# Optimization experiments

Hardware: AMD Instinct MI355X
Metric: run time of the kernel (lower is better)

The kernel has to match this reference:

```python
import jax, jax.numpy as jnp
import numpy as np

N = 100000   # nodes
E = 1600000  # edges
IN = 3       # in_channels
H = 32       # hidden_channels
C = 10       # num_classes_dynamic (== num output classes here)
G = 64       # number of graphs in the batch


def setup_inputs() -> dict:
    key = jax.random.key(0)
    ks = jax.random.split(key, 12)
    def w(k, shape, fan_in):
        return jax.random.normal(k, shape, jnp.float32) / np.sqrt(fan_in).astype(np.float32)
    inp = {}
    inp["x"] = jax.random.normal(ks[0], (N, IN), jnp.float32)
    inp["edge_index"] = jax.random.randint(ks[1], (2, E), 0, N, jnp.int32)
    inp["batch"] = jnp.sort(jax.random.randint(ks[2], (N,), 0, G, jnp.int32))
    # per-class linear filters (DynamicEdgeConv.filters)
    inp["filt_W"] = w(ks[3], (C, IN, H), IN)
    inp["filt_b"] = jnp.zeros((C, H), jnp.float32)
    # shared edge MLP: Linear(2H,H) -> ReLU -> Linear(H,H)
    inp["mlp_W1"] = w(ks[4], (2 * H, H), 2 * H)
    inp["mlp_b1"] = jnp.zeros((H,), jnp.float32)
    inp["mlp_W2"] = w(ks[5], (H, H), H)
    inp["mlp_b2"] = jnp.zeros((H,), jnp.float32)
    # GCN layers (gcn1 input dim hardcoded 323 = IN + C*H)
    inp["gcn1_W"] = w(ks[6], (IN + C * H, H), IN + C * H)
    inp["gcn1_b"] = jnp.zeros((H,), jnp.float32)
    inp["gcn2_W"] = w(ks[7], (H, H), H)
    inp["gcn2_b"] = jnp.zeros((H,), jnp.float32)
    # classifier
    inp["cls_W"] = w(ks[8], (H, C), H)
    inp["cls_b"] = jnp.zeros((C,), jnp.float32)
    return inp


def _gcn_conv(x, W, b, row, col, dinv):
    # PyG GCNConv: add self-loops, sym-normalize, aggregate src->dst
    xw = x @ W                                   # [N, H]
    norm = dinv[row] * dinv[col]                 # [E]
    out = jax.ops.segment_sum(xw[row] * norm[:, None], col, num_segments=x.shape[0])
    out = out + xw * (dinv * dinv)[:, None]      # self-loop term, norm = 1/deg_i
    return out + b


def _forward(x, edge_index, batch, filt_W, filt_b, mlp_W1, mlp_b1, mlp_W2, mlp_b2,
             gcn1_W, gcn1_b, gcn2_W, gcn2_b, cls_W, cls_b):
    row, col = edge_index[0], edge_index[1]
    n = x.shape[0]

    # DynamicEdgeConv: per-class filter -> gather(row,col) -> edge MLP -> scatter_add into col
    def per_class(_, wb):
        Wc, bc = wb
        xc = x @ Wc + bc                                      # [N, H]
        ef = jnp.concatenate([xc[row], xc[col]], axis=1)      # [E, 2H]
        h = jax.nn.relu(ef @ mlp_W1 + mlp_b1) @ mlp_W2 + mlp_b2
        return None, jax.ops.segment_sum(h, col, num_segments=n)
    _, aggs = jax.lax.scan(per_class, None, (filt_W, filt_b))  # [C, N, H]

    feat = jnp.concatenate([x, aggs.transpose(1, 0, 2).reshape(n, -1)], axis=1)  # [N, IN + C*H]

    deg = jax.ops.segment_sum(jnp.ones(row.shape[0], x.dtype), col, num_segments=n) + 1.0
    dinv = deg ** -0.5
    h1 = jax.nn.relu(_gcn_conv(feat, gcn1_W, gcn1_b, row, col, dinv))
    h2 = jax.nn.relu(_gcn_conv(h1, gcn2_W, gcn2_b, row, col, dinv))

    counts = jax.ops.segment_sum(jnp.ones(n, x.dtype), batch, num_segments=G)
    pooled = jax.ops.segment_sum(h2, batch, num_segments=G) / jnp.maximum(counts, 1.0)[:, None]
    return pooled @ cls_W + cls_b                             # [G, C]


def reference(x, edge_index, batch, filt_W, filt_b, mlp_W1, mlp_b1, mlp_W2, mlp_b2,
              gcn1_W, gcn1_b, gcn2_W, gcn2_b, cls_W, cls_b):
    return _forward(x, edge_index, batch, filt_W, filt_b, mlp_W1, mlp_b1, mlp_W2, mlp_b2,
                    gcn1_W, gcn1_b, gcn2_W, gcn2_b, cls_W, cls_b)
```

## Files before the change

kernel.cpp:

```cpp
#include <hip/hip_runtime.h>

#define NN 100000
#define NE 1600000
#define HH 32
#define CC 10
#define GG 64
#define NB 391
#define PBLK 100
#define ECH 16000
#define MTOT (NB * PBLK)
#define MSB ((MTOT + 255) / 256)

typedef _Float16 half8 __attribute__((ext_vector_type(8)));
typedef _Float16 half2v __attribute__((ext_vector_type(2)));
typedef float f32x4 __attribute__((ext_vector_type(4)));

__global__ void zero_f(float* p, int n) {
    int i = blockIdx.x * 256 + threadIdx.x;
    if (i < n) p[i] = 0.0f;
}

__global__ void precompute_small(const float* __restrict__ fW, const float* __restrict__ fb,
                                 const float* __restrict__ W1, const float* __restrict__ b1,
                                 const float* __restrict__ W2, const float* __restrict__ b2,
                                 const float* __restrict__ g1W, float* __restrict__ tab) {
    int c = blockIdx.x;
    int k = threadIdx.x >> 5;
    int j = threadIdx.x & 31;
    float m = 0.f;
    for (int mm = 0; mm < 32; ++mm)
        m += W2[k * 32 + mm] * g1W[(3 + 32 * c + mm) * 32 + j];
    tab[2240 + c * 1024 + k * 32 + j] = m;

    if (k < 3) {
        float a = 0.f, b = 0.f;
        for (int i = 0; i < 32; ++i) {
            float w = fW[c * 96 + k * 32 + i];
            a += w * W1[i * 32 + j];
            b += w * W1[(32 + i) * 32 + j];
        }
        tab[c * 96 + k * 32 + j] = a;
        tab[960 + c * 96 + k * 32 + j] = b;
    } else if (k == 3) {
        float h = b1[j];
        for (int i = 0; i < 32; ++i)
            h += fb[c * 32 + i] * (W1[i * 32 + j] + W1[(32 + i) * 32 + j]);
        tab[1920 + c * 32 + j] = h;
    } else if (k == 4 && c == 0) {
        float t = 0.f;
        for (int cc2 = 0; cc2 < CC; ++cc2)
            for (int mm = 0; mm < 32; ++mm)
                t += b2[mm] * g1W[(3 + 32 * cc2 + mm) * 32 + j];
        tab[12480 + j] = t;
    }
}

__global__ void mfrag_kernel(const float* __restrict__ tab, _Float16* __restrict__ Mfrag) {
    int gid = blockIdx.x * 256 + threadIdx.x;
    if (gid >= 1280) return;
    int set = gid >> 6, l = gid & 63;
    int kc = set >> 1, jt = set & 1;
    int j = jt * 16 + (l & 15);
    int kbase = kc * 32 + (l >> 4) * 8;
#pragma unroll
    for (int i = 0; i < 8; ++i)
        Mfrag[gid * 8 + i] = (_Float16)tab[2240 + (kbase + i) * 32 + j];
}

__global__ void bucket_hist(const int* __restrict__ ei, int* __restrict__ mat) {
    __shared__ int h[NB];
    int blk = blockIdx.x, tid = threadIdx.x;
    for (int i = tid; i < NB; i += 256) h[i] = 0;
    __syncthreads();
    int base = blk * ECH;
    for (int k = tid; k < ECH; k += 256)
        atomicAdd(&h[ei[NE + base + k] >> 8], 1);
    __syncthreads();
    for (int i = tid; i < NB; i += 256) mat[i * PBLK + blk] = h[i];
}

__global__ void scan_m1(const int* __restrict__ mat, int* __restrict__ msum) {
    __shared__ int sh[256];
    int b = blockIdx.x, t = threadIdx.x;
    int i = b * 256 + t;
    sh[t] = (i < MTOT) ? mat[i] : 0;
    __syncthreads();
    for (int off = 128; off > 0; off >>= 1) {
        if (t < off) sh[t] += sh[t + off];
        __syncthreads();
    }
    if (t == 0) msum[b] = sh[0];
}

__global__ void scan_m2(int* __restrict__ msum) {
    __shared__ int sh[256];
    int t = threadIdx.x;
    int v = (t < MSB) ? msum[t] : 0;
    sh[t] = v;
    __syncthreads();
    for (int off = 1; off < 256; off <<= 1) {
        int add = (t >= off) ? sh[t - off] : 0;
        __syncthreads();
        sh[t] += add;
        __syncthreads();
    }
    if (t < MSB) msum[t] = sh[t] - v;
}

__global__ void scan_m3(int* __restrict__ mat, const int* __restrict__ msum) {
    __shared__ int sh[256];
    int b = blockIdx.x, t = threadIdx.x;
    int i = b * 256 + t;
    int v = (i < MTOT) ? mat[i] : 0;
    sh[t] = v;
    __syncthreads();
    for (int off = 1; off < 256; off <<= 1) {
        int add = (t >= off) ? sh[t - off] : 0;
        __syncthreads();
        sh[t] += add;
        __syncthreads();
    }
    if (i < MTOT) mat[i] = sh[t] - v + msum[b];
}

__global__ void bucket_scatter(const int* __restrict__ ei, const int* __restrict__ mat,
                               unsigned int* __restrict__ part) {
    __shared__ int bas[NB];
    __shared__ int cur[NB];
    int blk = blockIdx.x, tid = threadIdx.x;
    for (int i = tid; i < NB; i += 256) { bas[i] = mat[i * PBLK + blk]; cur[i] = 0; }
    __syncthreads();
    int base = blk * ECH;
    for (int k = tid; k < ECH; k += 256) {
        int e = base + k;
        int r = ei[e];
        int c = ei[NE + e];
        int b = c >> 8;
        int local = atomicAdd(&cur[b], 1);
        part[bas[b] + local] = (unsigned)r | ((unsigned)(c & 255) << 24);
    }
}

__global__ void bucket_build(const unsigned int* __restrict__ part, const int* __restrict__ mat,
                             const float* __restrict__ x, int* __restrict__ csr_row,
                             int* __restrict__ ideg, int* __restrict__ offs,
                             float* __restrict__ dinv, float4* __restrict__ xpad) {
    __shared__ int lh[256];
    __shared__ int lex[256];
    __shared__ int cur[256];
    int b = blockIdx.x, tid = threadIdx.x;
    int ebase = mat[b * PBLK];
    int eend = (b == NB - 1) ? NE : mat[(b + 1) * PBLK];
    int m = eend - ebase;
    lh[tid] = 0;
    __syncthreads();
    for (int k = tid; k < m; k += 256) {
        unsigned v = part[ebase + k];
        atomicAdd(&lh[v >> 24], 1);
    }
    __syncthreads();
    int cnt = lh[tid];
    lex[tid] = cnt;
    __syncthreads();
    for (int off = 1; off < 256; off <<= 1) {
        int v = (tid >= off) ? lex[tid - off] : 0;
        __syncthreads();
        lex[tid] += v;
        __syncthreads();
    }
    int excl = lex[tid] - cnt;
    lex[tid] = excl;
    cur[tid] = 0;
    int n = b * 256 + tid;
    if (n < NN) {
        ideg[n] = cnt;
        offs[n] = ebase + excl;
        float di = rsqrtf((float)cnt + 1.0f);
        dinv[n] = di;
        xpad[n] = make_float4(x[n * 3], x[n * 3 + 1], x[n * 3 + 2], di);
    }
    if (b == 0 && tid == 0) offs[NN] = NE;
    __syncthreads();
    for (int k = tid; k < m; k += 256) {
        unsigned v = part[ebase + k];
        int cl = (int)(v >> 24);
        int r = (int)(v & 0x00FFFFFFu);
        int local = atomicAdd(&cur[cl], 1);
        csr_row[ebase + lex[cl] + local] = r;
    }
}

__device__ __forceinline__ float bcast_lane(float v, int t) {
    return __uint_as_float(__builtin_amdgcn_readlane(__float_as_uint(v), (unsigned)t));
}

__global__ __launch_bounds__(256, 8) void edgeconv_fused(
    const float4* __restrict__ xpad, const int* __restrict__ offs,
    const int* __restrict__ csr_row, const float* __restrict__ tab,
    _Float16* __restrict__ aggh) {
    int lane = threadIdx.x & 63;
    int j = lane & 31;
    int half = lane >> 5;
    int c0 = half * 5;

    float A0[5], A1[5], A2[5], B0[5], B1[5], B2[5], hb[5];
#pragma unroll
    for (int i = 0; i < 5; ++i) {
        int cb = (c0 + i) * 96;
        A0[i] = tab[cb + j];       A1[i] = tab[cb + 32 + j];       A2[i] = tab[cb + 64 + j];
        B0[i] = tab[960 + cb + j]; B1[i] = tab[960 + cb + 32 + j]; B2[i] = tab[960 + cb + 64 + j];
        hb[i] = tab[1920 + (c0 + i) * 32 + j];
    }

    int wid = blockIdx.x * 4 + (threadIdx.x >> 6);
    const int wstride = gridDim.x * 4;

    for (int n = wid; n < NN; n += wstride) {
        float4 xn = xpad[n];
        float va[5], acc[5];
#pragma unroll
        for (int i = 0; i < 5; ++i) {
            va[i] = hb[i] + xn.x * B0[i] + xn.y * B1[i] + xn.z * B2[i];
            acc[i] = 0.f;
        }
        int e0 = offs[n], e1 = offs[n + 1];
        for (int base = e0; base < e1; base += 64) {
            int ee = base + lane;
            int r = (ee < e1) ? csr_row[ee] : 0;
            float4 q = xpad[r];
            int cnt2 = e1 - base;
            if (cnt2 > 64) cnt2 = 64;
            int t = 0;
            for (; t + 1 < cnt2; t += 2) {
                float px0 = bcast_lane(q.x, t),     py0 = bcast_lane(q.y, t),     pz0 = bcast_lane(q.z, t);
                float px1 = bcast_lane(q.x, t + 1), py1 = bcast_lane(q.y, t + 1), pz1 = bcast_lane(q.z, t + 1);
#pragma unroll
                for (int i = 0; i < 5; ++i)
                    acc[i] += fmaxf(va[i] + px0 * A0[i] + py0 * A1[i] + pz0 * A2[i], 0.f);
#pragma unroll
                for (int i = 0; i < 5; ++i)
                    acc[i] += fmaxf(va[i] + px1 * A0[i] + py1 * A1[i] + pz1 * A2[i], 0.f);
            }
            if (t < cnt2) {
                float px = bcast_lane(q.x, t), py = bcast_lane(q.y, t), pz = bcast_lane(q.z, t);
#pragma unroll
                for (int i = 0; i < 5; ++i)
                    acc[i] += fmaxf(va[i] + px * A0[i] + py * A1[i] + pz * A2[i], 0.f);
            }
        }
        _Float16* arow = aggh + (size_t)n * 320 + half * 160 + j;
#pragma unroll
        for (int i = 0; i < 5; ++i) arow[i * 32] = (_Float16)acc[i];
    }
}

__global__ __launch_bounds__(256) void fold_mfma(
    const _Float16* __restrict__ aggh, const _Float16* __restrict__ MfragG,
    const float4* __restrict__ xpad, const int* __restrict__ ideg,
    const float* __restrict__ tab, const float* __restrict__ g1W,
    _Float16* __restrict__ y1) {
    __shared__ _Float16 Mf[10240];
    {
        const uint4* src = (const uint4*)MfragG;
        uint4* dst = (uint4*)Mf;
        for (int i = threadIdx.x; i < 1280; i += 256) dst[i] = src[i];
    }
    __syncthreads();

    int wave = blockIdx.x * 4 + (threadIdx.x >> 6);
    int lane = threadIdx.x & 63;
    int n0 = wave * 16;
    if (n0 >= NN) return;

    int m = lane & 15, q = lane >> 4;
    int arow_n = n0 + m;
    bool rowok = arow_n < NN;
    const _Float16* arow = aggh + (size_t)arow_n * 320 + q * 8;

    const half8* mf = (const half8*)Mf;
    f32x4 acc0 = {0.f, 0.f, 0.f, 0.f};
    f32x4 acc1 = {0.f, 0.f, 0.f, 0.f};

    for (int kc = 0; kc < 10; ++kc) {
        half8 a;
        if (rowok) a = *(const half8*)(arow + kc * 32);
        else {
#pragma unroll
            for (int i = 0; i < 8; ++i) a[i] = (_Float16)0.f;
        }
        half8 b0 = mf[(kc * 2 + 0) * 64 + lane];
        half8 b1 = mf[(kc * 2 + 1) * 64 + lane];
        acc0 = __builtin_amdgcn_mfma_f32_16x16x32_f16(a, b0, acc0, 0, 0, 0);
        acc1 = __builtin_amdgcn_mfma_f32_16x16x32_f16(a, b1, acc1, 0, 0, 0);
    }

    int jcol = lane & 15;
    float t0 = tab[12480 + jcol],      t1 = tab[12480 + 16 + jcol];
    float w00 = g1W[jcol],      w01 = g1W[32 + jcol],      w02 = g1W[64 + jcol];
    float w10 = g1W[16 + jcol], w11 = g1W[48 + jcol],      w12 = g1W[80 + jcol];
#pragma unroll
    for (int r = 0; r < 4; ++r) {
        int node = n0 + q * 4 + r;
        if (node < NN) {
            float4 xn = xpad[node];
            float dg = (float)ideg[node];
            float v0 = dg * t0 + xn.x * w00 + xn.y * w01 + xn.z * w02 + acc0[r];
            float v1 = dg * t1 + xn.x * w10 + xn.y * w11 + xn.z * w12 + acc1[r];
            y1[node * 32 + jcol]      = (_Float16)(v0 * xn.w);
            y1[node * 32 + 16 + jcol] = (_Float16)(v1 * xn.w);
        }
    }
}

__global__ __launch_bounds__(256, 8) void prop1_fused(
    const int* __restrict__ offs, const int* __restrict__ csr_row,
    const unsigned int* __restrict__ y1p, const float* __restrict__ dinv,
    const float* __restrict__ g1b, const float* __restrict__ g2W,
    unsigned int* __restrict__ y2p) {
    __shared__ float g2s[1024];
    for (int i = threadIdx.x; i < 1024; i += 256) g2s[i] = g2W[i];
    __syncthreads();

    int lane = threadIdx.x & 63;
    int l = lane & 15;
    int wid = blockIdx.x * 4 + (threadIdx.x >> 6);
    int n = wid * 4 + (lane >> 4);
    if (n >= NN) return;

    int e0 = offs[n], e1 = offs[n + 1];
    float sAl = 0.f, sAh = 0.f, sBl = 0.f, sBh = 0.f;
    int e = e0;
    for (; e + 7 < e1; e += 8) {
        int r[8];
#pragma unroll
        for (int u = 0; u < 8; ++u) r[u] = csr_row[e + u];
        half2v p[8];
#pragma unroll
        for (int u = 0; u < 8; ++u) p[u] = __builtin_bit_cast(half2v, y1p[r[u] * 16 + l]);
#pragma unroll
        for (int u = 0; u < 8; u += 2) {
            sAl += (float)p[u].x;     sAh += (float)p[u].y;
            sBl += (float)p[u + 1].x; sBh += (float)p[u + 1].y;
        }
    }
    for (; e < e1; ++e) {
        int r = csr_row[e];
        half2v p = __builtin_bit_cast(half2v, y1p[r * 16 + l]);
        sAl += (float)p.x; sAh += (float)p.y;
    }
    float di = dinv[n];
    half2v pn = __builtin_bit_cast(half2v, y1p[n * 16 + l]);
    float h1l = di * (sAl + sBl + (float)pn.x);
    float h1h = di * (sAh + sBh + (float)pn.y);
    float hl = fmaxf(h1l + g1b[2 * l], 0.f);
    float hh = fmaxf(h1h + g1b[2 * l + 1], 0.f);

    float al = 0.f, ah = 0.f;
    int base = lane & 48;
#pragma unroll
    for (int m = 0; m < 16; ++m) {
        float xl = __shfl(hl, base + m, 64);
        float xh2 = __shfl(hh, base + m, 64);
        al += xl * g2s[(2 * m) * 32 + 2 * l] + xh2 * g2s[(2 * m + 1) * 32 + 2 * l];
        ah += xl * g2s[(2 * m) * 32 + 2 * l + 1] + xh2 * g2s[(2 * m + 1) * 32 + 2 * l + 1];
    }
    half2v o = {(_Float16)(al * di), (_Float16)(ah * di)};
    y2p[n * 16 + l] = __builtin_bit_cast(unsigned int, o);
}

__global__ __launch_bounds__(256, 8) void prop2_plain(
    const int* __restrict__ offs, const int* __restrict__ csr_row,
    const unsigned int* __restrict__ y2p, const float* __restrict__ dinv,
    unsigned int* __restrict__ outp) {
    int lane = threadIdx.x & 63;
    int l = lane & 15;
    int wid = blockIdx.x * 4 + (threadIdx.x >> 6);
    int n = wid * 4 + (lane >> 4);
    if (n >= NN) return;

    int e0 = offs[n], e1 = offs[n + 1];
    float sAl = 0.f, sAh = 0.f, sBl = 0.f, sBh = 0.f;
    int e = e0;
    for (; e + 7 < e1; e += 8) {
        int r[8];
#pragma unroll
        for (int u = 0; u < 8; ++u) r[u] = csr_row[e + u];
        half2v p[8];
#pragma unroll
        for (int u = 0; u < 8; ++u) p[u] = __builtin_bit_cast(half2v, y2p[r[u] * 16 + l]);
#pragma unroll
        for (int u = 0; u < 8; u += 2) {
            sAl += (float)p[u].x;     sAh += (float)p[u].y;
            sBl += (float)p[u + 1].x; sBh += (float)p[u + 1].y;
        }
    }
    for (; e < e1; ++e) {
        int r = csr_row[e];
        half2v p = __builtin_bit_cast(half2v, y2p[r * 16 + l]);
        sAl += (float)p.x; sAh += (float)p.y;
    }
    float di = dinv[n];
    half2v pn = __builtin_bit_cast(half2v, y2p[n * 16 + l]);
    half2v o = {(_Float16)(di * (sAl + sBl + (float)pn.x)),
                (_Float16)(di * (sAh + sBh + (float)pn.y))};
    outp[n * 16 + l] = __builtin_bit_cast(unsigned int, o);
}

__global__ void pool_seg(const _Float16* __restrict__ h2, const float* __restrict__ g2b,
                         const int* __restrict__ batch, float* __restrict__ pooled,
                         float* __restrict__ counts) {
    int grp = threadIdx.x >> 5, j = threadIdx.x & 31;
    int base = (blockIdx.x * 8 + grp) * 64;
    if (base >= NN) return;
    float bj = g2b[j];
    float acc = 0.f, cnt = 0.f;
    int curg = -1;
    int lim = base + 64;
    if (lim > NN) lim = NN;
    for (int n = base; n < lim; ++n) {
        int g = batch[n];
        if (g != curg) {
            if (curg >= 0) {
                atomicAdd(&pooled[curg * 32 + j], acc);
                if (j == 0) atomicAdd(&counts[curg], cnt);
            }
            curg = g; acc = 0.f; cnt = 0.f;
        }
        acc += fmaxf((float)h2[n * 32 + j] + bj, 0.f);
        cnt += 1.f;
    }
    if (curg >= 0) {
        atomicAdd(&pooled[curg * 32 + j], acc);
        if (j == 0) atomicAdd(&counts[curg], cnt);
    }
}

__global__ void final_kernel(const float* __restrict__ pooled, const float* __restrict__ counts,
                             const float* __restrict__ clsW, const float* __restrict__ clsb,
                             float* __restrict__ out) {
    int tid = threadIdx.x;
    if (tid >= GG * CC) return;
    int g = tid / CC, cc = tid % CC;
    float inv = 1.0f / fmaxf(counts[g], 1.0f);
    float s = clsb[cc];
    for (int j = 0; j < 32; ++j) s += (pooled[g * 32 + j] * inv) * clsW[j * CC + cc];
    out[g * CC + cc] = s;
}

extern "C" void kernel_launch(void* const* d_in, const int* in_sizes, int n_in,
                              void* d_out, int out_size, void* d_ws, size_t ws_size,
                              hipStream_t stream) {
    const float* x     = (const float*)d_in[0];
    const int*   ei    = (const int*)d_in[1];
    const int*   batch = (const int*)d_in[2];
    const float* fW    = (const float*)d_in[3];
    const float* fb    = (const float*)d_in[4];
    const float* W1    = (const float*)d_in[5];
    const float* b1    = (const float*)d_in[6];
    const float* W2    = (const float*)d_in[7];
    const float* b2    = (const float*)d_in[8];
    const float* g1W   = (const float*)d_in[9];
    const float* g1b   = (const float*)d_in[10];
    const float* g2W   = (const float*)d_in[11];
    const float* g2b   = (const float*)d_in[12];
    const float* clsW  = (const float*)d_in[13];
    const float* clsb  = (const float*)d_in[14];
    float* out = (float*)d_out;

    float4*         xpad    = (float4*)d_ws;
    _Float16*       aggh    = (_Float16*)(xpad + NN);
    unsigned int*   part    = (unsigned int*)aggh;
    int*            csr_row = (int*)(aggh + (size_t)NN * 320);
    int*            mat     = (int*)(csr_row + NE);
    int*            msum    = mat + MTOT;
    int*            ideg    = msum + 256;
    int*            offs    = ideg + NN;
    float*          dinv    = (float*)(offs + NN + 1);
    float*          tab     = dinv + NN;
    _Float16*       Mfrag   = (_Float16*)(tab + 16384);
    _Float16*       y1      = Mfrag + 10240;
    unsigned int*   y2p     = (unsigned int*)(y1 + (size_t)NN * 32);
    unsigned int*   h2p     = y2p + (size_t)NN * 16;
    float*          pooled  = (float*)(h2p + (size_t)NN * 16);
    float*          counts  = pooled + GG * 32;

    const int propBlocks = (NN + 15) / 16;
    const int foldBlocks = ((NN + 15) / 16 + 3) / 4;

    zero_f<<<(GG * 33 + 255) / 256, 256, 0, stream>>>(pooled, GG * 33);
    precompute_small<<<10, 1024, 0, stream>>>(fW, fb, W1, b1, W2, b2, g1W, tab);
    mfrag_kernel<<<5, 256, 0, stream>>>(tab, Mfrag);

    bucket_hist<<<PBLK, 256, 0, stream>>>(ei, mat);
    scan_m1<<<MSB, 256, 0, stream>>>(mat, msum);
    scan_m2<<<1, 256, 0, stream>>>(msum);
    scan_m3<<<MSB, 256, 0, stream>>>(mat, msum);
    bucket_scatter<<<PBLK, 256, 0, stream>>>(ei, mat, part);
    bucket_build<<<NB, 256, 0, stream>>>(part, mat, x, csr_row, ideg, offs, dinv, xpad);

    edgeconv_fused<<<2048, 256, 0, stream>>>(xpad, offs, csr_row, tab, aggh);
    fold_mfma<<<foldBlocks, 256, 0, stream>>>(aggh, Mfrag, xpad, ideg, tab, g1W, y1);

    prop1_fused<<<propBlocks, 256, 0, stream>>>(offs, csr_row, (const unsigned int*)y1,
                                                dinv, g1b, g2W, y2p);
    prop2_plain<<<propBlocks, 256, 0, stream>>>(offs, csr_row, y2p, dinv, h2p);
    pool_seg<<<(NN + 511) / 512, 256, 0, stream>>>((const _Float16*)h2p, g2b, batch,
                                                   pooled, counts);
    final_kernel<<<1, 640, 0, stream>>>(pooled, counts, clsW, clsb, out);
}
```

Before: 399.7 us.

## Use packed fp16 math in edgeconv with half-wave edge splitting

Rewrites the edge-conv inner loop to run in packed half2 arithmetic, with two classes per register. The two half-waves now process alternate edges over all 10 classes, and their partial sums are combined with a cross-half shuffle at the end. A pre-broadcast fp16 copy of x is built in bucket_build, and the fp16 partial sums are flushed into fp32 accumulators every 8 steps to limit precision loss. This roughly halves the ALU instruction count per edge, at the cost of fp16 rounding in the pre-activation and accumulation, extra shuffles, and a lower occupancy hint.

Measured after the change: 391.5 us. 2.0% less time.

```diff
diff --git a/kernel.cpp b/kernel.cpp
--- a/kernel.cpp
+++ b/kernel.cpp
@@ -14,6 +14,8 @@
 typedef _Float16 half8 __attribute__((ext_vector_type(8)));
 typedef _Float16 half2v __attribute__((ext_vector_type(2)));
 typedef float f32x4 __attribute__((ext_vector_type(4)));
+
+__device__ __forceinline__ half2v bch(int v) { return __builtin_bit_cast(half2v, v); }
 
 __global__ void zero_f(float* p, int n) {
     int i = blockIdx.x * 256 + threadIdx.x;
@@ -144,7 +146,8 @@
 __global__ void bucket_build(const unsigned int* __restrict__ part, const int* __restrict__ mat,
                              const float* __restrict__ x, int* __restrict__ csr_row,
                              int* __restrict__ ideg, int* __restrict__ offs,
-                             float* __restrict__ dinv, float4* __restrict__ xpad) {
+                             float* __restrict__ dinv, float4* __restrict__ xpad,
+                             uint4* __restrict__ xs) {
     __shared__ int lh[256];
     __shared__ int lex[256];
     __shared__ int cur[256];
@@ -177,7 +180,13 @@
         offs[n] = ebase + excl;
         float di = rsqrtf((float)cnt + 1.0f);
         dinv[n] = di;
-        xpad[n] = make_float4(x[n * 3], x[n * 3 + 1], x[n * 3 + 2], di);
+        float x0 = x[n * 3], x1 = x[n * 3 + 1], x2 = x[n * 3 + 2];
+        xpad[n] = make_float4(x0, x1, x2, di);
+        _Float16 hx = (_Float16)x0, hy = (_Float16)x1, hz = (_Float16)x2;
+        half2v sx = {hx, hx}, sy = {hy, hy}, sz = {hz, hz};
+        xs[n] = make_uint4(__builtin_bit_cast(unsigned int, sx),
+                           __builtin_bit_cast(unsigned int, sy),
+                           __builtin_bit_cast(unsigned int, sz), 0u);
     }
     if (b == 0 && tid == 0) offs[NN] = NE;
     __syncthreads();
@@ -190,67 +199,101 @@
     }
 }
 
-__device__ __forceinline__ float bcast_lane(float v, int t) {
-    return __uint_as_float(__builtin_amdgcn_readlane(__float_as_uint(v), (unsigned)t));
-}
-
-__global__ __launch_bounds__(256, 8) void edgeconv_fused(
-    const float4* __restrict__ xpad, const int* __restrict__ offs,
+__global__ __launch_bounds__(256, 6) void edgeconv_fused(
+    const uint4* __restrict__ xs, const int* __restrict__ offs,
     const int* __restrict__ csr_row, const float* __restrict__ tab,
     _Float16* __restrict__ aggh) {
     int lane = threadIdx.x & 63;
     int j = lane & 31;
     int half = lane >> 5;
-    int c0 = half * 5;
-
-    float A0[5], A1[5], A2[5], B0[5], B1[5], B2[5], hb[5];
-#pragma unroll
-    for (int i = 0; i < 5; ++i) {
-        int cb = (c0 + i) * 96;
-        A0[i] = tab[cb + j];       A1[i] = tab[cb + 32 + j];       A2[i] = tab[cb + 64 + j];
-        B0[i] = tab[960 + cb + j]; B1[i] = tab[960 + cb + 32 + j]; B2[i] = tab[960 + cb + 64 + j];
-        hb[i] = tab[1920 + (c0 + i) * 32 + j];
-    }
+
+    half2v A0[5], A1[5], A2[5], B0[5], B1[5], B2[5], hb[5];
+#pragma unroll
+    for (int p = 0; p < 5; ++p) {
+        int c0 = 2 * p, c1 = 2 * p + 1;
+        A0[p] = half2v{(_Float16)tab[c0 * 96 + j],        (_Float16)tab[c1 * 96 + j]};
+        A1[p] = half2v{(_Float16)tab[c0 * 96 + 32 + j],   (_Float16)tab[c1 * 96 + 32 + j]};
+        A2[p] = half2v{(_Float16)tab[c0 * 96 + 64 + j],   (_Float16)tab[c1 * 96 + 64 + j]};
+        B0[p] = half2v{(_Float16)tab[960 + c0 * 96 + j],      (_Float16)tab[960 + c1 * 96 + j]};
+        B1[p] = half2v{(_Float16)tab[960 + c0 * 96 + 32 + j], (_Float16)tab[960 + c1 * 96 + 32 + j]};
+        B2[p] = half2v{(_Float16)tab[960 + c0 * 96 + 64 + j], (_Float16)tab[960 + c1 * 96 + 64 + j]};
+        hb[p] = half2v{(_Float16)tab[1920 + c0 * 32 + j], (_Float16)tab[1920 + c1 * 32 + j]};
+    }
+    const half2v zero = half2v{(_Float16)0.f, (_Float16)0.f};
 
     int wid = blockIdx.x * 4 + (threadIdx.x >> 6);
     const int wstride = gridDim.x * 4;
 
     for (int n = wid; n < NN; n += wstride) {
-        float4 xn = xpad[n];
-        float va[5], acc[5];
-#pragma unroll
-        for (int i = 0; i < 5; ++i) {
-            va[i] = hb[i] + xn.x * B0[i] + xn.y * B1[i] + xn.z * B2[i];
-            acc[i] = 0.f;
+        uint4 qn = xs[n];
+        half2v pxn = bch((int)qn.x), pyn = bch((int)qn.y), pzn = bch((int)qn.z);
+        half2v va[5];
+        float accf[10];
+#pragma unroll
+        for (int p = 0; p < 5; ++p) {
+            va[p] = hb[p] + pxn * B0[p] + pyn * B1[p] + pzn * B2[p];
+            accf[2 * p] = 0.f;
+            accf[2 * p + 1] = 0.f;
         }
         int e0 = offs[n], e1 = offs[n + 1];
         for (int base = e0; base < e1; base += 64) {
             int ee = base + lane;
             int r = (ee < e1) ? csr_row[ee] : 0;
-            float4 q = xpad[r];
-            int cnt2 = e1 - base;
-            if (cnt2 > 64) cnt2 = 64;
-            int t = 0;
-            for (; t + 1 < cnt2; t += 2) {
-                float px0 = bcast_lane(q.x, t),     py0 = bcast_lane(q.y, t),     pz0 = bcast_lane(q.z, t);
-                float px1 = bcast_lane(q.x, t + 1), py1 = bcast_lane(q.y, t + 1), pz1 = bcast_lane(q.z, t + 1);
-#pragma unroll
-                for (int i = 0; i < 5; ++i)
-                    acc[i] += fmaxf(va[i] + px0 * A0[i] + py0 * A1[i] + pz0 * A2[i], 0.f);
-#pragma unroll
-                for (int i = 0; i < 5; ++i)
-                    acc[i] += fmaxf(va[i] + px1 * A0[i] + py1 * A1[i] + pz1 * A2[i], 0.f);
+            uint4 q = xs[r];
+            int cnt = e1 - base;
+            if (cnt > 64) cnt = 64;
+            int tfull = cnt >> 1;
+            half2v acc[5];
+#pragma unroll
+            for (int p = 0; p < 5; ++p) acc[p] = zero;
+            for (int t = 0; t < tfull; ++t) {
+                int src = 2 * t + half;
+                half2v px = bch(__shfl((int)q.x, src, 64));
+                half2v py = bch(__shfl((int)q.y, src, 64));
+                half2v pz = bch(__shfl((int)q.z, src, 64));
+#pragma unroll
+                for (int p = 0; p < 5; ++p) {
+                    half2v u = va[p] + px * A0[p] + py * A1[p] + pz * A2[p];
+                    u = __builtin_elementwise_max(u, zero);
+                    acc[p] += u;
+                }
+                if ((t & 7) == 7) {
+#pragma unroll
+                    for (int p = 0; p < 5; ++p) {
+                        accf[2 * p]     += (float)acc[p].x;
+                        accf[2 * p + 1] += (float)acc[p].y;
+                        acc[p] = zero;
+                    }
+                }
             }
-            if (t < cnt2) {
-                float px = bcast_lane(q.x, t), py = bcast_lane(q.y, t), pz = bcast_lane(q.z, t);
-#pragma unroll
-                for (int i = 0; i < 5; ++i)
-                    acc[i] += fmaxf(va[i] + px * A0[i] + py * A1[i] + pz * A2[i], 0.f);
+            if (cnt & 1) {
+                int src = cnt - 1;
+                half2v px = bch(__shfl((int)q.x, src, 64));
+                half2v py = bch(__shfl((int)q.y, src, 64));
+                half2v pz = bch(__shfl((int)q.z, src, 64));
+                if (half == 0) {
+#pragma unroll
+                    for (int p = 0; p < 5; ++p) {
+                        half2v u = va[p] + px * A0[p] + py * A1[p] + pz * A2[p];
+                        u = __builtin_elementwise_max(u, zero);
+                        acc[p] += u;
+                    }
+                }
             }
-        }
-        _Float16* arow = aggh + (size_t)n * 320 + half * 160 + j;
-#pragma unroll
-        for (int i = 0; i < 5; ++i) arow[i * 32] = (_Float16)acc[i];
+#pragma unroll
+            for (int p = 0; p < 5; ++p) {
+                accf[2 * p]     += (float)acc[p].x;
+                accf[2 * p + 1] += (float)acc[p].y;
+            }
+        }
+#pragma unroll
+        for (int c = 0; c < 10; ++c) accf[c] += __shfl_xor(accf[c], 32, 64);
+        _Float16* arow = aggh + (size_t)n * 320 + j;
+#pragma unroll
+        for (int i = 0; i < 5; ++i) {
+            int c = half * 5 + i;
+            arow[c * 32] = (_Float16)accf[c];
+        }
     }
 }
 
@@ -468,7 +511,8 @@
     float* out = (float*)d_out;
 
     float4*         xpad    = (float4*)d_ws;
-    _Float16*       aggh    = (_Float16*)(xpad + NN);
+    uint4*          xs      = (uint4*)(xpad + NN);
+    _Float16*       aggh    = (_Float16*)(xs + NN);
     unsigned int*   part    = (unsigned int*)aggh;
     int*            csr_row = (int*)(aggh + (size_t)NN * 320);
     int*            mat     = (int*)(csr_row + NE);
@@ -496,9 +540,9 @@
     scan_m2<<<1, 256, 0, stream>>>(msum);
     scan_m3<<<MSB, 256, 0, stream>>>(mat, msum);
     bucket_scatter<<<PBLK, 256, 0, stream>>>(ei, mat, part);
-    bucket_build<<<NB, 256, 0, stream>>>(part, mat, x, csr_row, ideg, offs, dinv, xpad);
-
-    edgeconv_fused<<<2048, 256, 0, stream>>>(xpad, offs, csr_row, tab, aggh);
+    bucket_build<<<NB, 256, 0, stream>>>(part, mat, x, csr_row, ideg, offs, dinv, xpad, xs);
+
+    edgeconv_fused<<<2048, 256, 0, stream>>>(xs, offs, csr_row, tab, aggh);
     fold_mfma<<<foldBlocks, 256, 0, stream>>>(aggh, Mfrag, xpad, ideg, tab, g1W, y1);
 
     prop1_fused<<<propBlocks, 256, 0, stream>>>(offs, csr_row, (const unsigned int*)y1,
```
